# Kernel optimization log

Measured on AMD Instinct MI355X. Metric: run time of the kernel, lower is better.

Reference implementation:

```python
import jax, jax.numpy as jnp
import numpy as np

B, D_IN, D_H = 8192, 512, 1024


def setup_inputs() -> dict:
    key = jax.random.key(0)
    ks = jax.random.split(key, 5)
    # Kaiming-normal-ish init: std = sqrt(2/fan_in)
    Wx = jax.random.normal(ks[0], (D_IN, 4 * D_H), jnp.float32) * np.sqrt(2.0 / D_IN)
    Wh = jax.random.normal(ks[1], (D_H, 4 * D_H), jnp.float32) * np.sqrt(2.0 / D_H)
    b = jnp.zeros((4 * D_H,), jnp.float32)
    x = jax.random.normal(ks[2], (B, D_IN), jnp.float32)
    h = jax.random.normal(ks[3], (B, D_H), jnp.float32)
    c = jax.random.normal(ks[4], (B, D_H), jnp.float32)
    return {"x": x, "h": h, "c": c, "Wx": Wx, "Wh": Wh, "b": b}


def reference(x, h, c, Wx, Wh, b):
    # Fused gate pre-activations: [B, 4H] in gate order (g, i, f, o)
    gates = x @ Wx + h @ Wh + b[None, :]
    g_in, i_in, f_in, o_in = jnp.split(gates, 4, axis=-1)
    g_out = jnp.tanh(g_in)
    i_out = jax.nn.sigmoid(i_in)
    # NOTE: faithful to the original source's bug — f_out and o_out both use i_in.
    f_out = jax.nn.sigmoid(i_in)
    o_out = jax.nn.sigmoid(i_in)
    c_new = g_out * i_out + f_out * c
    h_new = jnp.tanh(c_new) * o_out
    return h_new, c_new
```

## Files before the change

### kernel.cpp

```cpp
#include <hip/hip_runtime.h>
#include <hip/hip_bf16.h>
#include <cstdint>

#define BROWS 8192
#define DIN   512
#define DH    1024
#define KTOT  1536
#define NT    (KTOT / 64)

typedef __bf16 bf16x8 __attribute__((ext_vector_type(8)));
typedef __bf16 bf16x4 __attribute__((ext_vector_type(4)));
typedef float  f32x4  __attribute__((ext_vector_type(4)));

__device__ __forceinline__ void load16_to_lds(const void* gptr, void* lptr) {
    __builtin_amdgcn_global_load_lds(
        (const __attribute__((address_space(1))) uint32_t*)gptr,
        (__attribute__((address_space(3))) uint32_t*)lptr,
        16, 0, 0);
}

__global__ __launch_bounds__(256) void cvtA_kernel(
    const float* __restrict__ x, const float* __restrict__ h,
    __bf16* __restrict__ A) {
    int t = blockIdx.x * 256 + threadIdx.x;
    int row = t / 192;
    int j = t - row * 192;
    int kg = j * 8;
    const float* src = (kg < DIN) ? (x + (size_t)row * DIN + kg)
                                  : (h + (size_t)row * DH + (kg - DIN));
    float4 u = *(const float4*)src;
    float4 v = *(const float4*)(src + 4);
    bf16x8 o = { (__bf16)u.x, (__bf16)u.y, (__bf16)u.z, (__bf16)u.w,
                 (__bf16)v.x, (__bf16)v.y, (__bf16)v.z, (__bf16)v.w };
    int swz = (j * 16) ^ ((row & 7) << 4);
    *(bf16x8*)((char*)A + (size_t)row * 3072 + swz) = o;
}

__global__ __launch_bounds__(256) void cvtB_kernel(
    const float* __restrict__ Wx, const float* __restrict__ Wh,
    __bf16* __restrict__ Bt) {
    __shared__ float tile[32][33];
    int k0 = blockIdx.x * 32;
    int n0 = blockIdx.y * 32;
    int tx = threadIdx.x;
    int ty = threadIdx.y;
#pragma unroll
    for (int i = 0; i < 4; ++i) {
        int k = k0 + ty + 8 * i;
        float v = (k < DIN) ? Wx[(size_t)k * 4096 + n0 + tx]
                            : Wh[(size_t)(k - DIN) * 4096 + n0 + tx];
        tile[ty + 8 * i][tx] = v;
    }
    __syncthreads();
    int n = n0 + tx;
    int kk = ty * 4;
    bf16x4 o = { (__bf16)tile[kk][tx], (__bf16)tile[kk + 1][tx],
                 (__bf16)tile[kk + 2][tx], (__bf16)tile[kk + 3][tx] };
    int swz = ((k0 + kk) * 2) ^ ((n & 7) << 4);
    *(bf16x4*)((char*)Bt + (size_t)n * 3072 + swz) = o;
}


#define BARRIER  do { __builtin_amdgcn_sched_barrier(0); __builtin_amdgcn_s_barrier(); __builtin_amdgcn_sched_barrier(0); } while (0)
#define VMW(n)   do { asm volatile("s_waitcnt vmcnt(" #n ")" ::: "memory"); __builtin_amdgcn_sched_barrier(0); } while (0)
#define LGKM0    do { asm volatile("s_waitcnt lgkmcnt(0)" ::: "memory"); __builtin_amdgcn_sched_barrier(0); } while (0)

#define STAGE_A(buf, mh, kt) do {                                              \
    const char* g0_ = Ab + (size_t)(brow + (mh) * 128 + r0) * 3072             \
                         + (size_t)(kt) * 128 + cb;                            \
    char* l0_ = sAb + (buf) * 32768 + ((mh) * 128 + r0) * 128 + cb;            \
    load16_to_lds(g0_, l0_);                                                   \
    load16_to_lds(g0_ + 64 * 3072, l0_ + 64 * 128);                            \
} while (0)

#define STAGE_B(buf, half, kt) do {                                            \
    const char* g0_ = Bb + (size_t)((half) * 1024 + bnp + r0) * 3072           \
                         + (size_t)(kt) * 128 + cb;                            \
    char* l0_ = sBb + (buf) * 32768 + ((half) * 128 + r0) * 128 + cb;          \
    load16_to_lds(g0_, l0_);                                                   \
    load16_to_lds(g0_ + 64 * 3072, l0_ + 64 * 128);                            \
} while (0)

#define READ_A(dst, c, mh)                                                     \
    _Pragma("unroll")                                                          \
    for (int m2_ = 0; m2_ < 2; ++m2_) {                                        \
        _Pragma("unroll")                                                      \
        for (int ks_ = 0; ks_ < 2; ++ks_) {                                    \
            int row_ = wrow + (mh) * 32 + m2_ * 16 + l15;                      \
            int kb_ = ks_ * 64 + l4x16;                                        \
            dst[m2_][ks_] = *(const bf16x8*)(sAb + (c) * 32768 + row_ * 128    \
                                             + (kb_ ^ swzkey));                \
        }                                                                      \
    }

#define READ_B(dst, c, half)                                                   \
    _Pragma("unroll")                                                          \
    for (int ni_ = 0; ni_ < 4; ++ni_) {                                        \
        _Pragma("unroll")                                                      \
        for (int ks_ = 0; ks_ < 2; ++ks_) {                                    \
            int row_ = (half) * 128 + wcol + ni_ * 16 + l15;                   \
            int kb_ = ks_ * 64 + l4x16;                                        \
            dst[ni_][ks_] = *(const bf16x8*)(sBb + (c) * 32768 + row_ * 128    \
                                             + (kb_ ^ swzkey));                \
        }                                                                      \
    }

#define MMA(ACC, MH, AF, BF) do {                                              \
    __builtin_amdgcn_s_setprio(1);                                             \
    _Pragma("unroll")                                                          \
    for (int ks_ = 0; ks_ < 2; ++ks_) {                                        \
        _Pragma("unroll")                                                      \
        for (int m2_ = 0; m2_ < 2; ++m2_) {                                    \
            _Pragma("unroll")                                                  \
            for (int ni_ = 0; ni_ < 4; ++ni_) {                                \
                ACC[(MH) * 2 + m2_][ni_] =                                     \
                    __builtin_amdgcn_mfma_f32_16x16x32_bf16(                   \
                        AF[m2_][ks_], BF[ni_][ks_], ACC[(MH) * 2 + m2_][ni_],  \
                        0, 0, 0);                                              \
            }                                                                  \
        }                                                                      \
    }                                                                          \
    __builtin_amdgcn_s_setprio(0);                                             \
    __builtin_amdgcn_sched_barrier(0);                                         \
} while (0)

__global__ __launch_bounds__(512, 2) void lstm_gemm_kernel(
    const __bf16* __restrict__ A,
    const __bf16* __restrict__ Bt,
    const float* __restrict__ bias,
    const float* __restrict__ c_in,
    float* __restrict__ out_h,
    float* __restrict__ out_c) {
    __shared__ __bf16 sA[2][256][64];
    __shared__ __bf16 sB[2][256][64];

    const int tid  = threadIdx.x;
    const int lane = tid & 63;
    const int wid  = tid >> 6;
    const int wr   = wid & 3;
    const int wc   = wid >> 2;
    const int bid  = blockIdx.x;
    const int bnp  = (bid & 7) * 128;
    const int brow = (bid >> 3) * 256;

    const int l15    = lane & 15;
    const int l4x16  = (lane >> 4) * 16;
    const int swzkey = (l15 & 7) << 4;
    const int wrow   = wr * 64;
    const int wcol   = wc * 64;

    const int r0 = tid >> 3;
    const int cb = (tid & 7) * 16;

    const char* Ab = (const char*)A;
    const char* Bb = (const char*)Bt;
    char* sAb = (char*)&sA[0][0][0];
    char* sBb = (char*)&sB[0][0][0];

    f32x4 accg[4][4], acci[4][4];
#pragma unroll
    for (int mi = 0; mi < 4; ++mi)
#pragma unroll
        for (int ni = 0; ni < 4; ++ni) {
            accg[mi][ni] = (f32x4){0.f, 0.f, 0.f, 0.f};
            acci[mi][ni] = (f32x4){0.f, 0.f, 0.f, 0.f};
        }

    bf16x8 aF0[2][2], aF1[2][2], bgF[4][2], biF[4][2];

    STAGE_A(0, 0, 0);
    STAGE_A(0, 1, 0);
    STAGE_B(0, 0, 0);
    STAGE_B(0, 1, 0);

    for (int t = 0; t < NT - 1; ++t) {
        const int c  = t & 1;
        const int nb = c ^ 1;
        VMW(2); BARRIER;
        READ_A(aF0, c, 0);
        READ_B(bgF, c, 0);
        STAGE_A(nb, 0, t + 1);
        BARRIER; LGKM0;
        MMA(accg, 0, aF0, bgF);
        BARRIER;
        READ_A(aF1, c, 1);
        STAGE_A(nb, 1, t + 1);
        BARRIER; LGKM0;
        MMA(accg, 1, aF1, bgF);
        VMW(4); BARRIER;
        READ_B(biF, c, 1);
        STAGE_B(nb, 0, t + 1);
        BARRIER; LGKM0;
        MMA(acci, 0, aF0, biF);
        BARRIER;
        STAGE_B(nb, 1, t + 1);
        BARRIER;
        MMA(acci, 1, aF1, biF);
    }
    {
        const int c = (NT - 1) & 1;
        VMW(2); BARRIER;
        READ_A(aF0, c, 0);
        READ_B(bgF, c, 0);
        BARRIER; LGKM0;
        MMA(accg, 0, aF0, bgF);
        BARRIER;
        READ_A(aF1, c, 1);
        BARRIER; LGKM0;
        MMA(accg, 1, aF1, bgF);
        VMW(0); BARRIER;
        READ_B(biF, c, 1);
        BARRIER; LGKM0;
        MMA(acci, 0, aF0, biF);
        MMA(acci, 1, aF1, biF);
    }

    const int R0 = brow + wrow;
    const int C0 = bnp + wcol;
    const int l4 = lane >> 4;
#pragma unroll
    for (int ni = 0; ni < 4; ++ni) {
        const int col = C0 + ni * 16 + l15;
        const float bg = bias[col];
        const float bi = bias[1024 + col];
#pragma unroll
        for (int mi = 0; mi < 4; ++mi) {
#pragma unroll
            for (int r = 0; r < 4; ++r) {
                const int row = R0 + mi * 16 + l4 * 4 + r;
                const float g_in = accg[mi][ni][r] + bg;
                const float i_in = acci[mi][ni][r] + bi;
                const float s  = 1.0f / (1.0f + __expf(-i_in));
                const float tg = 2.0f / (1.0f + __expf(-2.0f * g_in)) - 1.0f;
                const float cv = c_in[(size_t)row * DH + col];
                const float cn = s * (tg + cv);
                const float hn = (2.0f / (1.0f + __expf(-2.0f * cn)) - 1.0f) * s;
                out_h[(size_t)row * DH + col] = hn;
                out_c[(size_t)row * DH + col] = cn;
            }
        }
    }
}

extern "C" void kernel_launch(void* const* d_in, const int* in_sizes, int n_in,
                              void* d_out, int out_size, void* d_ws, size_t ws_size,
                              hipStream_t stream) {
    const float* x  = (const float*)d_in[0];
    const float* h  = (const float*)d_in[1];
    const float* c  = (const float*)d_in[2];
    const float* Wx = (const float*)d_in[3];
    const float* Wh = (const float*)d_in[4];
    const float* b  = (const float*)d_in[5];

    __bf16* A  = (__bf16*)d_ws;
    __bf16* Bt = (__bf16*)((char*)d_ws + (size_t)BROWS * KTOT * 2);

    float* out_h = (float*)d_out;
    float* out_c = out_h + (size_t)BROWS * DH;

    cvtA_kernel<<<(BROWS * (KTOT / 8)) / 256, 256, 0, stream>>>(x, h, A);
    cvtB_kernel<<<dim3(KTOT / 32, 2048 / 32), dim3(32, 8), 0, stream>>>(Wx, Wh, Bt);
    lstm_gemm_kernel<<<256, 512, 0, stream>>>(A, Bt, b, c, out_h, out_c);
}
```

Baseline: 82.42 us.

## Shrink GEMM block tile to 128x64 with XCD-aware band/panel block mapping

Reduces the per-block output tile from 256 rows x 128 cols (per gate) to 128 rows x 64 cols, launches 1024 blocks instead of 256, and raises launch bounds to 4 blocks per CU. Block indices are remapped so each XCD handles contiguous row bands, aiming at L2 reuse of A and B. The pipeline is simplified to two MMA phases per k-step with smaller LDS buffers. The intent is better CU utilisation and occupancy on the 256-CU part. The cost is lower arithmetic intensity per block and more redundant global loads of A and B.

```diff
diff --git a/kernel.cpp b/kernel.cpp
--- a/kernel.cpp
+++ b/kernel.cpp
@@ -65,58 +65,72 @@
 #define VMW(n)   do { asm volatile("s_waitcnt vmcnt(" #n ")" ::: "memory"); __builtin_amdgcn_sched_barrier(0); } while (0)
 #define LGKM0    do { asm volatile("s_waitcnt lgkmcnt(0)" ::: "memory"); __builtin_amdgcn_sched_barrier(0); } while (0)
 
-#define STAGE_A(buf, mh, kt) do {                                              \
-    const char* g0_ = Ab + (size_t)(brow + (mh) * 128 + r0) * 3072             \
+#define STAGE_A(buf, kt) do {                                                  \
+    const char* g0_ = Ab + (size_t)(brow + r0) * 3072                          \
                          + (size_t)(kt) * 128 + cb;                            \
-    char* l0_ = sAb + (buf) * 32768 + ((mh) * 128 + r0) * 128 + cb;            \
+    char* l0_ = sAb + (buf) * 16384 + r0 * 128 + cb;                           \
     load16_to_lds(g0_, l0_);                                                   \
     load16_to_lds(g0_ + 64 * 3072, l0_ + 64 * 128);                            \
 } while (0)
 
-#define STAGE_B(buf, half, kt) do {                                            \
-    const char* g0_ = Bb + (size_t)((half) * 1024 + bnp + r0) * 3072           \
+#define STAGE_BG(buf, kt) do {                                                 \
+    const char* g0_ = Bb + (size_t)(bnp + r0) * 3072                           \
                          + (size_t)(kt) * 128 + cb;                            \
-    char* l0_ = sBb + (buf) * 32768 + ((half) * 128 + r0) * 128 + cb;          \
-    load16_to_lds(g0_, l0_);                                                   \
-    load16_to_lds(g0_ + 64 * 3072, l0_ + 64 * 128);                            \
-} while (0)
-
-#define READ_A(dst, c, mh)                                                     \
+    load16_to_lds(g0_, sBb + (buf) * 16384 + r0 * 128 + cb);                   \
+} while (0)
+
+#define STAGE_BI(buf, kt) do {                                                 \
+    const char* g0_ = Bb + (size_t)(1024 + bnp + r0) * 3072                    \
+                         + (size_t)(kt) * 128 + cb;                            \
+    load16_to_lds(g0_, sBb + (buf) * 16384 + (64 + r0) * 128 + cb);            \
+} while (0)
+
+#define READ_A(dst, c)                                                         \
     _Pragma("unroll")                                                          \
     for (int m2_ = 0; m2_ < 2; ++m2_) {                                        \
         _Pragma("unroll")                                                      \
         for (int ks_ = 0; ks_ < 2; ++ks_) {                                    \
-            int row_ = wrow + (mh) * 32 + m2_ * 16 + l15;                      \
+            int row_ = wrow + m2_ * 16 + l15;                                  \
             int kb_ = ks_ * 64 + l4x16;                                        \
-            dst[m2_][ks_] = *(const bf16x8*)(sAb + (c) * 32768 + row_ * 128    \
+            dst[m2_][ks_] = *(const bf16x8*)(sAb + (c) * 16384 + row_ * 128    \
                                              + (kb_ ^ swzkey));                \
         }                                                                      \
     }
 
-#define READ_B(dst, c, half)                                                   \
-    _Pragma("unroll")                                                          \
-    for (int ni_ = 0; ni_ < 4; ++ni_) {                                        \
+#define READ_BG(dst, c)                                                        \
+    _Pragma("unroll")                                                          \
+    for (int ni_ = 0; ni_ < 2; ++ni_) {                                        \
         _Pragma("unroll")                                                      \
         for (int ks_ = 0; ks_ < 2; ++ks_) {                                    \
-            int row_ = (half) * 128 + wcol + ni_ * 16 + l15;                   \
+            int row_ = wcol + ni_ * 16 + l15;                                  \
             int kb_ = ks_ * 64 + l4x16;                                        \
-            dst[ni_][ks_] = *(const bf16x8*)(sBb + (c) * 32768 + row_ * 128    \
+            dst[ni_][ks_] = *(const bf16x8*)(sBb + (c) * 16384 + row_ * 128    \
                                              + (kb_ ^ swzkey));                \
         }                                                                      \
     }
 
-#define MMA(ACC, MH, AF, BF) do {                                              \
+#define READ_BI(dst, c)                                                        \
+    _Pragma("unroll")                                                          \
+    for (int ni_ = 0; ni_ < 2; ++ni_) {                                        \
+        _Pragma("unroll")                                                      \
+        for (int ks_ = 0; ks_ < 2; ++ks_) {                                    \
+            int row_ = 64 + wcol + ni_ * 16 + l15;                             \
+            int kb_ = ks_ * 64 + l4x16;                                        \
+            dst[ni_][ks_] = *(const bf16x8*)(sBb + (c) * 16384 + row_ * 128    \
+                                             + (kb_ ^ swzkey));                \
+        }                                                                      \
+    }
+
+#define MMA(ACC, AF, BF) do {                                                  \
     __builtin_amdgcn_s_setprio(1);                                             \
     _Pragma("unroll")                                                          \
     for (int ks_ = 0; ks_ < 2; ++ks_) {                                        \
         _Pragma("unroll")                                                      \
         for (int m2_ = 0; m2_ < 2; ++m2_) {                                    \
             _Pragma("unroll")                                                  \
-            for (int ni_ = 0; ni_ < 4; ++ni_) {                                \
-                ACC[(MH) * 2 + m2_][ni_] =                                     \
-                    __builtin_amdgcn_mfma_f32_16x16x32_bf16(                   \
-                        AF[m2_][ks_], BF[ni_][ks_], ACC[(MH) * 2 + m2_][ni_],  \
-                        0, 0, 0);                                              \
+            for (int ni_ = 0; ni_ < 2; ++ni_) {                                \
+                ACC[m2_][ni_] = __builtin_amdgcn_mfma_f32_16x16x32_bf16(       \
+                    AF[m2_][ks_], BF[ni_][ks_], ACC[m2_][ni_], 0, 0, 0);       \
             }                                                                  \
         }                                                                      \
     }                                                                          \
@@ -124,30 +138,35 @@
     __builtin_amdgcn_sched_barrier(0);                                         \
 } while (0)
 
-__global__ __launch_bounds__(512, 2) void lstm_gemm_kernel(
+__global__ __launch_bounds__(512, 4) void lstm_gemm_kernel(
     const __bf16* __restrict__ A,
     const __bf16* __restrict__ Bt,
     const float* __restrict__ bias,
     const float* __restrict__ c_in,
     float* __restrict__ out_h,
     float* __restrict__ out_c) {
-    __shared__ __bf16 sA[2][256][64];
-    __shared__ __bf16 sB[2][256][64];
+    __shared__ __bf16 sA[2][128][64];
+    __shared__ __bf16 sB[2][128][64];
 
     const int tid  = threadIdx.x;
     const int lane = tid & 63;
     const int wid  = tid >> 6;
     const int wr   = wid & 3;
     const int wc   = wid >> 2;
-    const int bid  = blockIdx.x;
-    const int bnp  = (bid & 7) * 128;
-    const int brow = (bid >> 3) * 256;
+
+    const int bid   = blockIdx.x;
+    const int xcd   = bid & 7;
+    const int idx   = bid >> 3;
+    const int band  = xcd * 8 + (idx & 7);
+    const int panel = idx >> 3;
+    const int brow  = band * 128;
+    const int bnp   = panel * 64;
 
     const int l15    = lane & 15;
     const int l4x16  = (lane >> 4) * 16;
     const int swzkey = (l15 & 7) << 4;
-    const int wrow   = wr * 64;
-    const int wcol   = wc * 64;
+    const int wrow   = wr * 32;
+    const int wcol   = wc * 32;
 
     const int r0 = tid >> 3;
     const int cb = (tid & 7) * 16;
@@ -157,74 +176,60 @@
     char* sAb = (char*)&sA[0][0][0];
     char* sBb = (char*)&sB[0][0][0];
 
-    f32x4 accg[4][4], acci[4][4];
-#pragma unroll
-    for (int mi = 0; mi < 4; ++mi)
-#pragma unroll
-        for (int ni = 0; ni < 4; ++ni) {
+    f32x4 accg[2][2], acci[2][2];
+#pragma unroll
+    for (int mi = 0; mi < 2; ++mi)
+#pragma unroll
+        for (int ni = 0; ni < 2; ++ni) {
             accg[mi][ni] = (f32x4){0.f, 0.f, 0.f, 0.f};
             acci[mi][ni] = (f32x4){0.f, 0.f, 0.f, 0.f};
         }
 
-    bf16x8 aF0[2][2], aF1[2][2], bgF[4][2], biF[4][2];
-
-    STAGE_A(0, 0, 0);
-    STAGE_A(0, 1, 0);
-    STAGE_B(0, 0, 0);
-    STAGE_B(0, 1, 0);
+    bf16x8 aF[2][2], bgF[2][2], biF[2][2];
+
+    STAGE_A(0, 0);
+    STAGE_BG(0, 0);
+    STAGE_BI(0, 0);
 
     for (int t = 0; t < NT - 1; ++t) {
         const int c  = t & 1;
         const int nb = c ^ 1;
+        VMW(1); BARRIER;
+        READ_A(aF, c);
+        READ_BG(bgF, c);
+        STAGE_A(nb, t + 1);
+        BARRIER; LGKM0;
+        MMA(accg, aF, bgF);
         VMW(2); BARRIER;
-        READ_A(aF0, c, 0);
-        READ_B(bgF, c, 0);
-        STAGE_A(nb, 0, t + 1);
-        BARRIER; LGKM0;
-        MMA(accg, 0, aF0, bgF);
-        BARRIER;
-        READ_A(aF1, c, 1);
-        STAGE_A(nb, 1, t + 1);
-        BARRIER; LGKM0;
-        MMA(accg, 1, aF1, bgF);
-        VMW(4); BARRIER;
-        READ_B(biF, c, 1);
-        STAGE_B(nb, 0, t + 1);
-        BARRIER; LGKM0;
-        MMA(acci, 0, aF0, biF);
-        BARRIER;
-        STAGE_B(nb, 1, t + 1);
-        BARRIER;
-        MMA(acci, 1, aF1, biF);
+        READ_BI(biF, c);
+        STAGE_BG(nb, t + 1);
+        STAGE_BI(nb, t + 1);
+        BARRIER; LGKM0;
+        MMA(acci, aF, biF);
     }
     {
         const int c = (NT - 1) & 1;
-        VMW(2); BARRIER;
-        READ_A(aF0, c, 0);
-        READ_B(bgF, c, 0);
-        BARRIER; LGKM0;
-        MMA(accg, 0, aF0, bgF);
-        BARRIER;
-        READ_A(aF1, c, 1);
-        BARRIER; LGKM0;
-        MMA(accg, 1, aF1, bgF);
+        VMW(1); BARRIER;
+        READ_A(aF, c);
+        READ_BG(bgF, c);
+        BARRIER; LGKM0;
+        MMA(accg, aF, bgF);
         VMW(0); BARRIER;
-        READ_B(biF, c, 1);
-        BARRIER; LGKM0;
-        MMA(acci, 0, aF0, biF);
-        MMA(acci, 1, aF1, biF);
+        READ_BI(biF, c);
+        BARRIER; LGKM0;
+        MMA(acci, aF, biF);
     }
 
     const int R0 = brow + wrow;
     const int C0 = bnp + wcol;
     const int l4 = lane >> 4;
 #pragma unroll
-    for (int ni = 0; ni < 4; ++ni) {
+    for (int ni = 0; ni < 2; ++ni) {
         const int col = C0 + ni * 16 + l15;
         const float bg = bias[col];
         const float bi = bias[1024 + col];
 #pragma unroll
-        for (int mi = 0; mi < 4; ++mi) {
+        for (int mi = 0; mi < 2; ++mi) {
 #pragma unroll
             for (int r = 0; r < 4; ++r) {
                 const int row = R0 + mi * 16 + l4 * 4 + r;
@@ -260,5 +265,5 @@
 
     cvtA_kernel<<<(BROWS * (KTOT / 8)) / 256, 256, 0, stream>>>(x, h, A);
     cvtB_kernel<<<dim3(KTOT / 32, 2048 / 32), dim3(32, 8), 0, stream>>>(Wx, Wh, Bt);
-    lstm_gemm_kernel<<<256, 512, 0, stream>>>(A, Bt, b, c, out_h, out_c);
-}
+    lstm_gemm_kernel<<<1024, 512, 0, stream>>>(A, Bt, b, c, out_h, out_c);
+}
```

Result: slower. 84.37 us (+2.4%).
